# Kernel optimization log

Measured on AMD Instinct MI355X. Metric: run time of the kernel, lower is better.

Reference implementation:

```python
import jax, jax.numpy as jnp
import numpy as np

SR = 44100
B, T = 4, SR * 3          # batch, samples (duration_secs=3)
NWT, L = 64, 512          # n_wavetables, wavetable_len


def setup_inputs() -> dict:
    key = jax.random.key(0)
    k1, k2, k3, k4, k5 = jax.random.split(key, 5)
    pitch = jax.random.uniform(k1, (B, T, 1), dtype=jnp.float32, minval=50.0, maxval=500.0)
    amplitude = jax.random.uniform(k2, (B, T, 1), dtype=jnp.float32)
    y = jax.random.normal(k3, (B, T), dtype=jnp.float32)
    wavetables = jax.random.normal(k4, (NWT, L), dtype=jnp.float32) * 0.01
    # replicate init: last sample equals first sample of each table
    wavetables = wavetables.at[:, -1].set(wavetables[:, 0])
    conv_w = jax.random.normal(k5, (1, 1, 5), dtype=jnp.float32) * 0.3  # Conv1d(1,1,5)
    conv_b = jnp.zeros((1,), dtype=jnp.float32)
    return {"pitch": pitch, "amplitude": amplitude, "y": y,
            "wavetables": wavetables, "conv_w": conv_w, "conv_b": conv_b,
            "duration_secs": 3}


def reference(pitch, amplitude, y, wavetables, conv_w, conv_b, duration_secs):
    Lwt = wavetables.shape[1]
    freq = pitch.squeeze(-1)                                   # (B, T)
    increment = freq / SR * Lwt                                # (B, T)
    # NOTE: faithful to source: subtract batch-row 0 from every row
    index = jnp.cumsum(increment, axis=1) - increment[0]
    index = index % Lwt
    idx_low = jnp.floor(index)
    idx_high = jnp.ceil(index)
    alpha = index - idx_low                                    # (B, T)
    il = idx_low.astype(jnp.int32)
    ih = idx_high.astype(jnp.int32) % Lwt
    # vectorized over all 64 wavetables at once (source loops in Python)
    low = jnp.take(wavetables, il, axis=1)                     # (N, B, T)
    high = jnp.take(wavetables, ih, axis=1)                    # (N, B, T)
    waveforms = low + alpha * (high - low)                     # (N, B, T)
    # attention: mean over batch of waveform * y
    att = jnp.mean(waveforms * y, axis=1)                      # (N, T)
    att = jax.lax.conv_general_dilated(
        att[:, None, :], conv_w, window_strides=(1,), padding=[(2, 2)],
        dimension_numbers=("NCH", "OIH", "NCH"))[:, 0, :] + conv_b[0]
    att = jax.nn.softmax(att, axis=0)                          # softmax over wavetables
    out = jnp.einsum("nbt,nt->bt", waveforms, att)             # (B, T)
    out = out[..., None] * amplitude                           # (B, T, 1)
    return out
```

## Files before the change

### kernel.cpp

```cpp
#include <hip/hip_runtime.h>
#include <math.h>

#define LWT 512
#define NWT 64
#define BB 4
#define SBASE 16
#define TPW 60
#define WPB 4
#define TPB (TPW * WPB)
#define WSTRIDE 17


#define INC_C ((float)(512.0 / 44100.0))

__device__ __forceinline__ float inc_mul(float p) {
  float v = p * INC_C;
  asm volatile("" : "+v"(v));
  return v;
}
__device__ __forceinline__ float inc_of(const float* p, int t) { return inc_mul(p[t]); }

__global__ void __launch_bounds__(256) scan_level0(const float* __restrict__ pitch,
                                                   float* __restrict__ sarr,
                                                   float* __restrict__ s1g,
                                                   const float* __restrict__ wt,
                                                   float* __restrict__ wtT,
                                                   int T, int NB1) {
  if (blockIdx.y == BB) {
    int i = blockIdx.x * blockDim.x + threadIdx.x;
    if (i < NWT * LWT) {
      int n = i >> 9, c = i & 511;
      wtT[c * NWT + n] = wt[i];
    }
    return;
  }
  int k = blockIdx.x * blockDim.x + threadIdx.x;
  int b = blockIdx.y;
  if (k >= NB1) return;
  const float* prow = pitch + (size_t)b * T;
  float* srow = sarr + (size_t)b * T;
  int t0 = k * SBASE;
  float run = 0.0f;
  if (t0 + SBASE <= T) {
    const float4* p4 = reinterpret_cast<const float4*>(prow + t0);
    float4* s4o = reinterpret_cast<float4*>(srow + t0);
#pragma unroll
    for (int i = 0; i < 4; ++i) {
      float4 v = p4[i];
      float4 o;
      run += inc_mul(v.x); o.x = run;
      run += inc_mul(v.y); o.y = run;
      run += inc_mul(v.z); o.z = run;
      run += inc_mul(v.w); o.w = run;
      s4o[i] = o;
    }
  } else {
    for (int t = t0; t < T; ++t) { run += inc_of(prow, t); srow[t] = run; }
  }
  s1g[(size_t)b * NB1 + k] = run;
}

__global__ void __launch_bounds__(1024) scan_mid(float* __restrict__ s1g,
                                                 float* __restrict__ s2g,
                                                 int NB1, int NB2) {
  int b = blockIdx.x, tid = threadIdx.x;
  float* s1r = s1g + (size_t)b * NB1;
  __shared__ float s2[544];
  __shared__ float s3[48];
  __shared__ float s4[16];
  const int NB3 = (NB2 + SBASE - 1) / SBASE;
  const int NB4 = (NB3 + SBASE - 1) / SBASE;
  if (tid < NB2) {
    int a0 = tid * SBASE, a1 = a0 + SBASE < NB1 ? a0 + SBASE : NB1;
    float run = 0.0f;
    for (int a = a0; a < a1; ++a) { run += s1r[a]; s1r[a] = run; }
    s2[tid] = run;
  }
  __syncthreads();
  if (tid < NB3) {
    int a0 = tid * SBASE, a1 = a0 + SBASE < NB2 ? a0 + SBASE : NB2;
    float run = 0.0f;
    for (int a = a0; a < a1; ++a) { run += s2[a]; s2[a] = run; }
    s3[tid] = run;
  }
  __syncthreads();
  if (tid < NB4) {
    int a0 = tid * SBASE, a1 = a0 + SBASE < NB3 ? a0 + SBASE : NB3;
    float run = 0.0f;
    for (int a = a0; a < a1; ++a) { run += s3[a]; s3[a] = run; }
    s4[tid] = run;
  }
  __syncthreads();
  if (tid == 0) { float r = 0.0f; for (int a = 0; a < NB4; ++a) { r += s4[a]; s4[a] = r; } }
  __syncthreads();
  if (tid < NB3 && tid >= SBASE) s3[tid] = s3[tid] + s4[tid / SBASE - 1];
  __syncthreads();
  if (tid < NB2) {
    float v = s2[tid];
    if (tid >= SBASE) v = v + s3[tid / SBASE - 1];
    s2g[(size_t)b * NB2 + tid] = v;
  }
}

__global__ void __launch_bounds__(256) fused_out(
    const float* __restrict__ pitch, const float* __restrict__ sarr,
    const float* __restrict__ s1g, const float* __restrict__ s2g,
    const float* __restrict__ y, const float* __restrict__ amp,
    const float* __restrict__ wtT, const float* __restrict__ cw,
    const float* __restrict__ cb, float* __restrict__ out,
    int T, int NB1, int NB2) {
  __shared__ float lds_wt[513 * WSTRIDE];
  int wid = threadIdx.x >> 6, lane = threadIdx.x & 63;
  int tw = blockIdx.x * TPB + wid * TPW;
  int t = tw - 2 + lane;

  bool valid = (t >= 0 && t < T);
  int loi0 = 0, loi1 = 0, loi2 = 0, loi3 = 0;
  float alf[BB] = {0.f, 0.f, 0.f, 0.f};
  float yv[BB] = {0.f, 0.f, 0.f, 0.f};
  float av[BB] = {0.f, 0.f, 0.f, 0.f};
  if (valid) {
#pragma unroll
    for (int b = 0; b < BB; ++b) {
      float S = sarr[(size_t)b * T + t];
      if (t >= SBASE) {
        int k1 = (t >> 4) - 1;
        float s1v = s1g[b * NB1 + k1];
        if (k1 >= SBASE) s1v = s1v + s2g[b * NB2 + (k1 >> 4) - 1];
        S = S + s1v;
      }
      float iv = S - inc_of(pitch, t);
      float q = iv * (1.0f / 512.0f);
      float k = floorf(q);
      iv = fmaf(-k, 512.0f, iv);
      float fl = floorf(iv);
      float alpha = iv - fl;
      int ili = (int)fl; if (ili > 511) ili = 511;
      int lo = ili * WSTRIDE;
      if (b == 0) loi0 = lo;
      else if (b == 1) loi1 = lo;
      else if (b == 2) loi2 = lo;
      else loi3 = lo;
      alf[b] = alpha;
      yv[b] = y[(size_t)b * T + t];
      av[b] = amp[(size_t)b * T + t];
    }
  }

  float w0 = cw[0], w1 = cw[1], w2 = cw[2], w3 = cw[3], w4 = cw[4];
  float bias = cb[0];
  float r0 = 0.f, r1 = 0.f, r2 = 0.f, r3 = 0.f, ssum = 0.f;

  for (int h = 0; h < 4; ++h) {
    __syncthreads();
    {
      const float4* w4p = reinterpret_cast<const float4*>(wtT);
      for (int idx = threadIdx.x; idx < 513 * 4; idx += 256) {
        int c = idx >> 2, k = idx & 3;
        int csrc = (c == 512) ? 0 : c;
        float4 v = w4p[csrc * 16 + h * 4 + k];
        int base = c * WSTRIDE + k * 4;
        lds_wt[base + 0] = v.x;
        lds_wt[base + 1] = v.y;
        lds_wt[base + 2] = v.z;
        lds_wt[base + 3] = v.w;
      }
    }
    __syncthreads();
#pragma unroll
    for (int n = 0; n < 16; ++n) {
      int b0 = loi0 + n, b1 = loi1 + n, b2 = loi2 + n, b3 = loi3 + n;
      float lo0 = lds_wt[b0], hi0 = lds_wt[b0 + WSTRIDE];
      float lo1 = lds_wt[b1], hi1 = lds_wt[b1 + WSTRIDE];
      float lo2 = lds_wt[b2], hi2 = lds_wt[b2 + WSTRIDE];
      float lo3 = lds_wt[b3], hi3 = lds_wt[b3 + WSTRIDE];
      float wv0 = lo0 + alf[0] * (hi0 - lo0);
      float wv1 = lo1 + alf[1] * (hi1 - lo1);
      float wv2 = lo2 + alf[2] * (hi2 - lo2);
      float wv3 = lo3 + alf[3] * (hi3 - lo3);
      float acc = wv0 * yv[0];
      acc += wv1 * yv[1];
      acc += wv2 * yv[2];
      acc += wv3 * yv[3];
      acc *= 0.25f;
      float am2 = __shfl(acc, lane - 2);
      float am1 = __shfl(acc, lane - 1);
      float ap1 = __shfl(acc, lane + 1);
      float ap2 = __shfl(acc, lane + 2);
      float c0 = bias + am2 * w0 + am1 * w1 + acc * w2 + ap1 * w3 + ap2 * w4;
      float e = __expf(c0);
      r0 += e * wv0;
      r1 += e * wv1;
      r2 += e * wv2;
      r3 += e * wv3;
      ssum += e;
    }
  }

  if (lane >= 2 && lane < 62 && t < T) {
#if __has_builtin(__builtin_amdgcn_rcpf)
    float rc = __builtin_amdgcn_rcpf(ssum);
#else
    float rc = 1.0f / ssum;
#endif
    out[(size_t)0 * T + t] = r0 * rc * av[0];
    out[(size_t)1 * T + t] = r1 * rc * av[1];
    out[(size_t)2 * T + t] = r2 * rc * av[2];
    out[(size_t)3 * T + t] = r3 * rc * av[3];
  }
}

extern "C" void kernel_launch(void* const* d_in, const int* in_sizes, int n_in,
                              void* d_out, int out_size, void* d_ws, size_t ws_size,
                              hipStream_t stream) {
  const float* pitch = (const float*)d_in[0];
  const float* amp   = (const float*)d_in[1];
  const float* y     = (const float*)d_in[2];
  const float* wt    = (const float*)d_in[3];
  const float* cw    = (const float*)d_in[4];
  const float* cb    = (const float*)d_in[5];
  float* out = (float*)d_out;

  int BT = in_sizes[2];
  int T = BT / BB;
  int NB1 = (T + SBASE - 1) / SBASE;
  int NB2 = (NB1 + SBASE - 1) / SBASE;

  float* ws   = (float*)d_ws;
  float* sarr = ws;
  float* wtT  = ws + (size_t)BT;
  float* s1g  = ws + (size_t)BT + NWT * LWT;
  float* s2g  = s1g + (size_t)BB * NB1;

  hipLaunchKernelGGL(scan_level0, dim3(128, BB + 1), dim3(256), 0, stream,
                     pitch, sarr, s1g, wt, wtT, T, NB1);
  hipLaunchKernelGGL(scan_mid, dim3(BB), dim3(1024), 0, stream, s1g, s2g, NB1, NB2);
  hipLaunchKernelGGL(fused_out, dim3((T + TPB - 1) / TPB), dim3(256), 0, stream,
                     pitch, sarr, s1g, s2g, y, amp, wtT, cw, cb, out, T, NB1, NB2);
}
```

Before: 54.20 us.

## Restructure fused kernel with precomputed lo/delta LDS pairs and DPP neighbour shifts

Drops the transposed-wavetable pass and has the fused kernel stage each group of 8 wavetables straight from the original layout into LDS as (low, high-low) float2 pairs. Each lookup then needs one 8-byte load and one FMA instead of two loads, a subtract and an FMA. Cross-lane shuffles for the conv stencil are replaced by chained DPP row shifts with a causal offset. The launch becomes a fixed grid of 256 blocks of 9 waves, and amplitude is loaded only at the store. The DPP row-shift edge handling is intricate and may not match the shuffle semantics across 16-lane row boundaries; the fixed grid also changes how many times each block restages the tables.

```diff
diff --git a/kernel.cpp b/kernel.cpp
--- a/kernel.cpp
+++ b/kernel.cpp
@@ -5,10 +5,9 @@
 #define NWT 64
 #define BB 4
 #define SBASE 16
-#define TPW 60
-#define WPB 4
-#define TPB (TPW * WPB)
-#define WSTRIDE 17
+#define WAVES 9
+#define THREADS (WAVES * 64)
+#define PSTRIDE 18
 
 
 #define INC_C ((float)(512.0 / 44100.0))
@@ -23,17 +22,7 @@
 __global__ void __launch_bounds__(256) scan_level0(const float* __restrict__ pitch,
                                                    float* __restrict__ sarr,
                                                    float* __restrict__ s1g,
-                                                   const float* __restrict__ wt,
-                                                   float* __restrict__ wtT,
                                                    int T, int NB1) {
-  if (blockIdx.y == BB) {
-    int i = blockIdx.x * blockDim.x + threadIdx.x;
-    if (i < NWT * LWT) {
-      int n = i >> 9, c = i & 511;
-      wtT[c * NWT + n] = wt[i];
-    }
-    return;
-  }
   int k = blockIdx.x * blockDim.x + threadIdx.x;
   int b = blockIdx.y;
   if (k >= NB1) return;
@@ -102,48 +91,55 @@
   }
 }
 
-__global__ void __launch_bounds__(256) fused_out(
+__device__ __forceinline__ float shdn1(float x, bool edge) {
+  int xi = __float_as_int(x);
+  int a = __builtin_amdgcn_update_dpp(0, xi, 0x111, 0xf, 0xf, true);
+  int b = __builtin_amdgcn_update_dpp(0, xi, 0x142, 0xf, 0xf, true);
+  return __int_as_float(edge ? b : a);
+}
+
+__global__ void __launch_bounds__(THREADS) fused_out(
     const float* __restrict__ pitch, const float* __restrict__ sarr,
     const float* __restrict__ s1g, const float* __restrict__ s2g,
     const float* __restrict__ y, const float* __restrict__ amp,
-    const float* __restrict__ wtT, const float* __restrict__ cw,
+    const float* __restrict__ wt, const float* __restrict__ cw,
     const float* __restrict__ cb, float* __restrict__ out,
     int T, int NB1, int NB2) {
-  __shared__ float lds_wt[513 * WSTRIDE];
+  __shared__ float lds_pairs[512 * PSTRIDE];
   int wid = threadIdx.x >> 6, lane = threadIdx.x & 63;
-  int tw = blockIdx.x * TPB + wid * TPW;
-  int t = tw - 2 + lane;
-
-  bool valid = (t >= 0 && t < T);
+  const bool edge = (lane & 15) == 0;
+  int seg = wid * 256 + blockIdx.x;
+  const int NSEG = (T + 59) / 60;
+  bool segv = seg < NSEG;
+  int ta = seg * 60 - 2 + lane;
+
   int loi0 = 0, loi1 = 0, loi2 = 0, loi3 = 0;
   float alf[BB] = {0.f, 0.f, 0.f, 0.f};
   float yv[BB] = {0.f, 0.f, 0.f, 0.f};
-  float av[BB] = {0.f, 0.f, 0.f, 0.f};
-  if (valid) {
+  if (segv && ta >= 0 && ta < T) {
 #pragma unroll
     for (int b = 0; b < BB; ++b) {
-      float S = sarr[(size_t)b * T + t];
-      if (t >= SBASE) {
-        int k1 = (t >> 4) - 1;
+      float S = sarr[(size_t)b * T + ta];
+      if (ta >= SBASE) {
+        int k1 = (ta >> 4) - 1;
         float s1v = s1g[b * NB1 + k1];
         if (k1 >= SBASE) s1v = s1v + s2g[b * NB2 + (k1 >> 4) - 1];
         S = S + s1v;
       }
-      float iv = S - inc_of(pitch, t);
+      float iv = S - inc_of(pitch, ta);
       float q = iv * (1.0f / 512.0f);
       float k = floorf(q);
       iv = fmaf(-k, 512.0f, iv);
       float fl = floorf(iv);
       float alpha = iv - fl;
       int ili = (int)fl; if (ili > 511) ili = 511;
-      int lo = ili * WSTRIDE;
+      int lo = ili * PSTRIDE;
       if (b == 0) loi0 = lo;
       else if (b == 1) loi1 = lo;
       else if (b == 2) loi2 = lo;
       else loi3 = lo;
       alf[b] = alpha;
-      yv[b] = y[(size_t)b * T + t];
-      av[b] = amp[(size_t)b * T + t];
+      yv[b] = y[(size_t)b * T + ta];
     }
   }
 
@@ -151,62 +147,66 @@
   float bias = cb[0];
   float r0 = 0.f, r1 = 0.f, r2 = 0.f, r3 = 0.f, ssum = 0.f;
 
-  for (int h = 0; h < 4; ++h) {
+  for (int h = 0; h < 8; ++h) {
     __syncthreads();
-    {
-      const float4* w4p = reinterpret_cast<const float4*>(wtT);
-      for (int idx = threadIdx.x; idx < 513 * 4; idx += 256) {
-        int c = idx >> 2, k = idx & 3;
-        int csrc = (c == 512) ? 0 : c;
-        float4 v = w4p[csrc * 16 + h * 4 + k];
-        int base = c * WSTRIDE + k * 4;
-        lds_wt[base + 0] = v.x;
-        lds_wt[base + 1] = v.y;
-        lds_wt[base + 2] = v.z;
-        lds_wt[base + 3] = v.w;
+    for (int idx = threadIdx.x; idx < 512 * 8; idx += THREADS) {
+      int nl = idx >> 9;
+      int c = idx & 511;
+      int ng = h * 8 + nl;
+      float lo = wt[ng * 512 + c];
+      float hi = wt[ng * 512 + ((c + 1) & 511)];
+      *reinterpret_cast<float2*>(&lds_pairs[c * PSTRIDE + 2 * nl]) =
+          make_float2(lo, hi - lo);
+    }
+    __syncthreads();
+    if (segv) {
+#pragma unroll
+      for (int nl = 0; nl < 8; ++nl) {
+        float2 p0 = *reinterpret_cast<const float2*>(&lds_pairs[loi0 + 2 * nl]);
+        float2 p1 = *reinterpret_cast<const float2*>(&lds_pairs[loi1 + 2 * nl]);
+        float2 p2 = *reinterpret_cast<const float2*>(&lds_pairs[loi2 + 2 * nl]);
+        float2 p3 = *reinterpret_cast<const float2*>(&lds_pairs[loi3 + 2 * nl]);
+        float wv0 = fmaf(alf[0], p0.y, p0.x);
+        float wv1 = fmaf(alf[1], p1.y, p1.x);
+        float wv2 = fmaf(alf[2], p2.y, p2.x);
+        float wv3 = fmaf(alf[3], p3.y, p3.x);
+        float acc = wv0 * yv[0];
+        acc += wv1 * yv[1];
+        acc += wv2 * yv[2];
+        acc += wv3 * yv[3];
+        acc *= 0.25f;
+        float d1 = shdn1(acc, edge);
+        float d2 = shdn1(d1, edge);
+        float d3 = shdn1(d2, edge);
+        float d4 = shdn1(d3, edge);
+        float c0 = bias + d4 * w0 + d3 * w1 + d2 * w2 + d1 * w3 + acc * w4;
+        float e = __expf(c0);
+        float s0 = shdn1(shdn1(wv0, edge), edge);
+        float s1 = shdn1(shdn1(wv1, edge), edge);
+        float s2 = shdn1(shdn1(wv2, edge), edge);
+        float s3 = shdn1(shdn1(wv3, edge), edge);
+        r0 += e * s0;
+        r1 += e * s1;
+        r2 += e * s2;
+        r3 += e * s3;
+        ssum += e;
       }
     }
-    __syncthreads();
-#pragma unroll
-    for (int n = 0; n < 16; ++n) {
-      int b0 = loi0 + n, b1 = loi1 + n, b2 = loi2 + n, b3 = loi3 + n;
-      float lo0 = lds_wt[b0], hi0 = lds_wt[b0 + WSTRIDE];
-      float lo1 = lds_wt[b1], hi1 = lds_wt[b1 + WSTRIDE];
-      float lo2 = lds_wt[b2], hi2 = lds_wt[b2 + WSTRIDE];
-      float lo3 = lds_wt[b3], hi3 = lds_wt[b3 + WSTRIDE];
-      float wv0 = lo0 + alf[0] * (hi0 - lo0);
-      float wv1 = lo1 + alf[1] * (hi1 - lo1);
-      float wv2 = lo2 + alf[2] * (hi2 - lo2);
-      float wv3 = lo3 + alf[3] * (hi3 - lo3);
-      float acc = wv0 * yv[0];
-      acc += wv1 * yv[1];
-      acc += wv2 * yv[2];
-      acc += wv3 * yv[3];
-      acc *= 0.25f;
-      float am2 = __shfl(acc, lane - 2);
-      float am1 = __shfl(acc, lane - 1);
-      float ap1 = __shfl(acc, lane + 1);
-      float ap2 = __shfl(acc, lane + 2);
-      float c0 = bias + am2 * w0 + am1 * w1 + acc * w2 + ap1 * w3 + ap2 * w4;
-      float e = __expf(c0);
-      r0 += e * wv0;
-      r1 += e * wv1;
-      r2 += e * wv2;
-      r3 += e * wv3;
-      ssum += e;
-    }
-  }
-
-  if (lane >= 2 && lane < 62 && t < T) {
+  }
+
+  if (segv && lane >= 4) {
+    int tout = ta - 2;
+    if (tout < T) {
 #if __has_builtin(__builtin_amdgcn_rcpf)
-    float rc = __builtin_amdgcn_rcpf(ssum);
+      float rc = __builtin_amdgcn_rcpf(ssum);
 #else
-    float rc = 1.0f / ssum;
+      float rc = 1.0f / ssum;
 #endif
-    out[(size_t)0 * T + t] = r0 * rc * av[0];
-    out[(size_t)1 * T + t] = r1 * rc * av[1];
-    out[(size_t)2 * T + t] = r2 * rc * av[2];
-    out[(size_t)3 * T + t] = r3 * rc * av[3];
+      out[(size_t)0 * T + tout] = r0 * rc * amp[(size_t)0 * T + tout];
+      out[(size_t)1 * T + tout] = r1 * rc * amp[(size_t)1 * T + tout];
+      out[(size_t)2 * T + tout] = r2 * rc * amp[(size_t)2 * T + tout];
+      out[(size_t)3 * T + tout] = r3 * rc * amp[(size_t)3 * T + tout];
+    }
   }
 }
 
@@ -228,13 +228,12 @@
 
   float* ws   = (float*)d_ws;
   float* sarr = ws;
-  float* wtT  = ws + (size_t)BT;
-  float* s1g  = ws + (size_t)BT + NWT * LWT;
+  float* s1g  = ws + (size_t)BT;
   float* s2g  = s1g + (size_t)BB * NB1;
 
-  hipLaunchKernelGGL(scan_level0, dim3(128, BB + 1), dim3(256), 0, stream,
-                     pitch, sarr, s1g, wt, wtT, T, NB1);
+  hipLaunchKernelGGL(scan_level0, dim3((NB1 + 255) / 256, BB), dim3(256), 0, stream,
+                     pitch, sarr, s1g, T, NB1);
   hipLaunchKernelGGL(scan_mid, dim3(BB), dim3(1024), 0, stream, s1g, s2g, NB1, NB2);
-  hipLaunchKernelGGL(fused_out, dim3((T + TPB - 1) / TPB), dim3(256), 0, stream,
-                     pitch, sarr, s1g, s2g, y, amp, wtT, cw, cb, out, T, NB1, NB2);
-}
+  hipLaunchKernelGGL(fused_out, dim3(256), dim3(THREADS), 0, stream,
+                     pitch, sarr, s1g, s2g, y, amp, wt, cw, cb, out, T, NB1, NB2);
+}
```

After: 57.80 us. +6.6%, slower.
